# Performance work log

Measured on AMD Instinct MI355X. Metric: run time of the kernel, lower is better.

## Reference

```python
import jax, jax.numpy as jnp
import numpy as np

N_NODES = 100000
N_EDGES = 3200000
NFEAT = 256
NHID = 256
NOUT = 128


def setup_inputs() -> dict:
    key = jax.random.key(0)
    ks = jax.random.split(key, 8)
    stdv1 = 1.0 / np.sqrt(NHID)
    stdv2 = 1.0 / np.sqrt(NOUT)
    return {
        "feat": jax.random.normal(ks[0], (N_NODES, NFEAT), dtype=jnp.float32),
        "row": jax.random.randint(ks[1], (N_EDGES,), 0, N_NODES, dtype=jnp.int32),
        "col": jax.random.randint(ks[2], (N_EDGES,), 0, N_NODES, dtype=jnp.int32),
        "edge_weight": jax.random.uniform(ks[3], (N_EDGES,), dtype=jnp.float32),
        "W1": jax.random.uniform(ks[4], (NFEAT, NHID), jnp.float32, -stdv1, stdv1),
        "b1": jax.random.uniform(ks[5], (NHID,), jnp.float32, -stdv1, stdv1),
        "W2": jax.random.uniform(ks[6], (NHID, NOUT), jnp.float32, -stdv2, stdv2),
        "b2": jax.random.uniform(ks[7], (NOUT,), jnp.float32, -stdv2, stdv2),
    }


def _spmm(row, col, edge_weight, x, n_nodes):
    # sparse.mm(adj, x): out[i] = sum_e w[e] * x[col[e]] for row[e] == i
    msgs = x[col] * edge_weight[:, None]  # [E, F] gather + scale
    return jax.ops.segment_sum(msgs, row, num_segments=n_nodes)


def reference(feat, row, col, edge_weight, W1, b1, W2, b2):
    # Layer 1: GraphConvolution + ReLU (dropout is identity in eval mode)
    h = _spmm(row, col, edge_weight, feat @ W1, feat.shape[0]) + b1
    h = jax.nn.relu(h)
    # Layer 2: GraphConvolution (no activation on final layer)
    out = _spmm(row, col, edge_weight, h @ W2, feat.shape[0]) + b2
    return out
```

## Files before the change

### kernel.cpp

```cpp
#include <hip/hip_runtime.h>
#include <hip/hip_bf16.h>

#define M_NODES 100000
#define E_EDGES 3200000
#define NBUCK 196
#define BSHIFT 9
#define BCAP 24576
#define K3_EPB 8192
#define K3_BLOCKS 391
#define TILESM 391

typedef __attribute__((ext_vector_type(8))) short short8;
typedef __attribute__((ext_vector_type(4))) float f32x4;
typedef __attribute__((ext_vector_type(2))) float f32x2;

__device__ inline unsigned short f2bf(float f) {
  __hip_bfloat16 h = __float2bfloat16(f);
  return __builtin_bit_cast(unsigned short, h);
}

#if __has_builtin(__builtin_amdgcn_cvt_pk_f32_fp8) && __has_builtin(__builtin_amdgcn_cvt_pk_fp8_f32)
#define HW_FP8 1
#endif

#ifndef HW_FP8
__device__ inline float fp8_dec1(unsigned int b) {
  const unsigned int s = (b >> 7) & 1u, e = (b >> 3) & 15u, m = b & 7u;
  float v;
  if (e == 0) v = (float)m * 0.001953125f;
  else v = __uint_as_float(((e + 120u) << 23) | (m << 20));
  return s ? -v : v;
}
__device__ inline unsigned int fp8_enc1(float x) {
  const unsigned int sb = (__float_as_uint(x) >> 31) << 7;
  float ax = fminf(fabsf(x), 448.f);
  if (ax < 0.0009765625f) return sb;
  const unsigned int xb = __float_as_uint(ax);
  const int ef = (int)(xb >> 23) - 127;
  if (ef < -6) {
    unsigned int m = (unsigned int)(ax * 512.f + 0.5f);
    if (m > 7u) return sb | 0x08u;
    return sb | m;
  }
  unsigned int m3 = ((xb & 0x7FFFFFu) + 0x80000u) >> 20;
  unsigned int e4 = (unsigned int)(ef + 7);
  if (m3 == 8u) { m3 = 0u; e4 += 1u; }
  if (e4 >= 16u) { e4 = 15u; m3 = 6u; }
  return sb | (e4 << 3) | m3;
}
#endif

__device__ inline void fp8x4_dec(unsigned int v, float* o) {
#ifdef HW_FP8
  const f32x2 lo = __builtin_amdgcn_cvt_pk_f32_fp8((int)v, false);
  const f32x2 hi = __builtin_amdgcn_cvt_pk_f32_fp8((int)v, true);
  o[0] = lo[0]; o[1] = lo[1]; o[2] = hi[0]; o[3] = hi[1];
#else
  o[0] = fp8_dec1(v & 255u); o[1] = fp8_dec1((v >> 8) & 255u);
  o[2] = fp8_dec1((v >> 16) & 255u); o[3] = fp8_dec1(v >> 24);
#endif
}
__device__ inline unsigned short fp8x2_enc(float a, float b) {
#ifdef HW_FP8
  const int p = __builtin_amdgcn_cvt_pk_fp8_f32(a, b, 0, false);
  return (unsigned short)(p & 0xFFFF);
#else
  return (unsigned short)(fp8_enc1(a) | (fp8_enc1(b) << 8));
#endif
}

__device__ inline unsigned int epk_col(unsigned int p) { return p >> 15; }
__device__ inline float epk_w(unsigned int p) {
  return __uint_as_float((p & 0x7FFFu) << 16);
}

__device__ inline void pack_one(const float* __restrict__ W,
                                unsigned short* __restrict__ Bf,
                                int idx, int N) {
  const int lane = idx & 63;
  const int f = idx >> 6;
  const int ntile = f % (N >> 4);
  const int kstep = f / (N >> 4);
  const int k0 = (kstep << 5) + ((lane >> 4) << 3);
  const int n = (ntile << 4) + (lane & 15);
  ushort4 lo, hi;
  lo.x = f2bf(W[(size_t)(k0 + 0) * N + n]);
  lo.y = f2bf(W[(size_t)(k0 + 1) * N + n]);
  lo.z = f2bf(W[(size_t)(k0 + 2) * N + n]);
  lo.w = f2bf(W[(size_t)(k0 + 3) * N + n]);
  hi.x = f2bf(W[(size_t)(k0 + 4) * N + n]);
  hi.y = f2bf(W[(size_t)(k0 + 5) * N + n]);
  hi.z = f2bf(W[(size_t)(k0 + 6) * N + n]);
  hi.w = f2bf(W[(size_t)(k0 + 7) * N + n]);
  *(ushort4*)&Bf[(size_t)idx * 8] = lo;
  *(ushort4*)&Bf[(size_t)idx * 8 + 4] = hi;
}

__global__ __launch_bounds__(512) void prep_fused(
    const int* __restrict__ row, const int* __restrict__ col,
    const float* __restrict__ w, int* __restrict__ bcnt,
    int2* __restrict__ P,
    const float* __restrict__ W1, const float* __restrict__ W2,
    unsigned short* __restrict__ W1f, unsigned short* __restrict__ W2f)
{
  __shared__ int2 stage[K3_EPB];
  __shared__ unsigned char sb[K3_EPB];
  __shared__ int hist[NBUCK], cur[NBUCK], delta[NBUCK];
  __shared__ int buf[256];
  const int t = threadIdx.x;

  if (blockIdx.x >= K3_BLOCKS) {
    const int pb = blockIdx.x - K3_BLOCKS;
    if (pb < 16) pack_one(W1, W1f, pb * 512 + t, 256);
    else         pack_one(W2, W2f, (pb - 16) * 512 + t, 128);
    return;
  }

  const int e0 = blockIdx.x * K3_EPB;
  const int e1 = min(e0 + K3_EPB, E_EDGES);
  if (t < NBUCK) hist[t] = 0;
  __syncthreads();
  for (int i = e0 + t; i < e1; i += 512)
    atomicAdd(&hist[row[i] >> BSHIFT], 1);
  __syncthreads();
  int v = 0;
  if (t < 256) {
    v = (t < NBUCK) ? hist[t] : 0;
    buf[t] = v;
  }
  __syncthreads();
  for (int d = 1; d < 256; d <<= 1) {
    int x = 0;
    if (t < 256 && t >= d) x = buf[t - d];
    __syncthreads();
    if (t < 256) buf[t] += x;
    __syncthreads();
  }
  if (t < NBUCK) {
    const int excl = buf[t] - hist[t];
    cur[t] = excl;
    const int g = atomicAdd(&bcnt[t], hist[t]);
    delta[t] = (t * BCAP + g) - excl;
  }
  __syncthreads();
  for (int i = e0 + t; i < e1; i += 512) {
    const int r = row[i];
    const int b = r >> BSHIFT;
    const int pos = atomicAdd(&cur[b], 1);
    stage[pos] = make_int2(col[i] | ((r & 511) << 20), __float_as_int(w[i]));
    sb[pos] = (unsigned char)b;
  }
  __syncthreads();
  const int n = e1 - e0;
  for (int i = t; i < n; i += 512)
    P[delta[sb[i]] + i] = stage[i];
}

__global__ __launch_bounds__(512) void csr_gemm1_fused(
    const int* __restrict__ bcnt, const int2* __restrict__ P,
    int* __restrict__ offs, unsigned int* __restrict__ epk,
    const float* __restrict__ A_, const unsigned short* __restrict__ Bf,
    unsigned char* __restrict__ C)
{
  __shared__ __align__(16) char smem[8 * 16 * 132 * 4];
  const int t = threadIdx.x;

  if (blockIdx.x < NBUCK) {
    int* buf   = (int*)smem;
    int* rhist = buf + 256;
    int* rcur  = rhist + 512;
    int* wsum  = rcur + 512;
    const int b = blockIdx.x;
    if (t < 256) buf[t] = (t < NBUCK) ? bcnt[t] : 0;
    __syncthreads();
    for (int d = 1; d < 256; d <<= 1) {
      int x = 0;
      if (t < 256 && t >= d) x = buf[t - d];
      __syncthreads();
      if (t < 256) buf[t] += x;
      __syncthreads();
    }
    const int cnt = bcnt[b];
    const int dst0 = buf[b] - cnt;
    const int src0 = b * BCAP;
    const int row0 = b << BSHIFT;
    if (b == 0 && t == 0) offs[M_NODES] = E_EDGES;
    __syncthreads();
    rhist[t] = 0;
    __syncthreads();
    for (int i = t; i < cnt; i += 512)
      atomicAdd(&rhist[(P[src0 + i].x >> 20) & 511], 1);
    __syncthreads();
    const int lane = t & 63, wv = t >> 6;
    const int v = rhist[t];
    int inc = v;
#pragma unroll
    for (int d = 1; d < 64; d <<= 1) {
      const int x = __shfl_up(inc, d);
      if (lane >= d) inc += x;
    }
    if (lane == 63) wsum[wv] = inc;
    __syncthreads();
    if (t < 8) {
      int sv = wsum[t];
#pragma unroll
      for (int d = 1; d < 8; d <<= 1) {
        const int x = __shfl_up(sv, d);
        if ((int)t >= d) sv += x;
      }
      wsum[t] = sv;
    }
    __syncthreads();
    const int excl = (wv ? wsum[wv - 1] : 0) + inc - v;
    const int gofs = dst0 + excl;
    if (row0 + t < M_NODES) offs[row0 + t] = gofs;
    rcur[t] = gofs;
    __syncthreads();
    for (int i = t; i < cnt; i += 512) {
      const int2 p = P[src0 + i];
      const int rl = (p.x >> 20) & 511;
      const int pos = atomicAdd(&rcur[rl], 1);
      const unsigned int wb = (unsigned int)f2bf(__int_as_float(p.y));
      epk[pos] = (((unsigned int)p.x & 0xFFFFFu) << 15) | wb;
    }
    return;
  }

  float (*cbuf)[16][132] = reinterpret_cast<float (*)[16][132]>(smem);
  const int bm = blockIdx.x - NBUCK;
  const int wv = t >> 6, lane = t & 63;
  const int m0 = (bm << 8) + ((wv & 3) << 6);
  const int n0 = (wv >> 2) << 7;
  const int rif = lane & 15, kg = lane >> 4;

  f32x4 acc[4][8] = {};

#pragma unroll
  for (int ks = 0; ks < 8; ++ks) {
    const int k0 = (ks << 5) + (kg << 3);
    short8 bfr[8];
    const size_t fbase = ((size_t)(ks << 4) + (n0 >> 4)) * 64 + lane;
#pragma unroll
    for (int nf = 0; nf < 8; ++nf)
      bfr[nf] = *(const short8*)&Bf[(fbase + (size_t)nf * 64) * 8];

    short8 afr[4];
#pragma unroll
    for (int mi = 0; mi < 4; ++mi) {
      const int row = m0 + (mi << 4) + rif;
      if (row < M_NODES) {
        const float* ap = &A_[(size_t)row * 256 + k0];
        const float4 lo = *(const float4*)ap;
        const float4 hi = *(const float4*)(ap + 4);
        short8 tt;
        tt[0] = (short)f2bf(lo.x); tt[1] = (short)f2bf(lo.y);
        tt[2] = (short)f2bf(lo.z); tt[3] = (short)f2bf(lo.w);
        tt[4] = (short)f2bf(hi.x); tt[5] = (short)f2bf(hi.y);
        tt[6] = (short)f2bf(hi.z); tt[7] = (short)f2bf(hi.w);
        afr[mi] = tt;
      } else {
        afr[mi] = (short8)0;
      }
    }
#pragma unroll
    for (int mi = 0; mi < 4; ++mi)
#pragma unroll
      for (int nf = 0; nf < 8; ++nf)
        acc[mi][nf] = __builtin_amdgcn_mfma_f32_16x16x32_bf16(
            afr[mi], bfr[nf], acc[mi][nf], 0, 0, 0);
  }

#pragma unroll
  for (int mi = 0; mi < 4; ++mi) {
#pragma unroll
    for (int nf = 0; nf < 8; ++nf) {
#pragma unroll
      for (int r = 0; r < 4; ++r)
        cbuf[wv][(kg << 2) + r][(nf << 4) + rif] = acc[mi][nf][r];
    }
    __syncthreads();
#pragma unroll
    for (int r = 0; r < 16; ++r) {
      const int row = m0 + (mi << 4) + r;
      if (row < M_NODES) {
        const float2 v = *(const float2*)&cbuf[wv][r][lane << 1];
        *(unsigned short*)&C[(size_t)row * 256 + n0 + (lane << 1)] =
            fp8x2_enc(v.x, v.y);
      }
    }
    __syncthreads();
  }
}

__global__ __launch_bounds__(256) void gemm2_mfma(
    const unsigned short* __restrict__ A_, const unsigned short* __restrict__ Bf,
    unsigned char* __restrict__ C)
{
  __shared__ float cbuf[4][16][132];
  const int wv = threadIdx.x >> 6, lane = threadIdx.x & 63;
  const int m0 = (blockIdx.x << 8) + (wv << 6);
  const int rif = lane & 15, kg = lane >> 4;

  f32x4 acc[4][8] = {};

#pragma unroll
  for (int ks = 0; ks < 8; ++ks) {
    const int k0 = (ks << 5) + (kg << 3);
    short8 bfr[8];
    const size_t fbase = ((size_t)(ks << 3)) * 64 + lane;
#pragma unroll
    for (int nf = 0; nf < 8; ++nf)
      bfr[nf] = *(const short8*)&Bf[(fbase + (size_t)nf * 64) * 8];

    short8 afr[4];
#pragma unroll
    for (int mi = 0; mi < 4; ++mi) {
      const int row = m0 + (mi << 4) + rif;
      afr[mi] = (row < M_NODES)
          ? *(const short8*)&A_[(size_t)row * 256 + k0]
          : (short8)0;
    }
#pragma unroll
    for (int mi = 0; mi < 4; ++mi)
#pragma unroll
      for (int nf = 0; nf < 8; ++nf)
        acc[mi][nf] = __builtin_amdgcn_mfma_f32_16x16x32_bf16(
            afr[mi], bfr[nf], acc[mi][nf], 0, 0, 0);
  }

#pragma unroll
  for (int mi = 0; mi < 4; ++mi) {
#pragma unroll
    for (int nf = 0; nf < 8; ++nf) {
#pragma unroll
      for (int r = 0; r < 4; ++r)
        cbuf[wv][(kg << 2) + r][(nf << 4) + rif] = acc[mi][nf][r];
    }
    __syncthreads();
#pragma unroll
    for (int r = 0; r < 16; ++r) {
      const int row = m0 + (mi << 4) + r;
      if (row < M_NODES) {
        const float2 v = *(const float2*)&cbuf[wv][r][lane << 1];
        *(unsigned short*)&C[(size_t)row * 128 + (lane << 1)] =
            fp8x2_enc(v.x, v.y);
      }
    }
    __syncthreads();
  }
}

__global__ __launch_bounds__(256) void spmm1_fused(
    const int* __restrict__ offs, const unsigned int* __restrict__ epk,
    const unsigned char* __restrict__ X, const float* __restrict__ b1,
    unsigned short* __restrict__ Hb)
{
  const int w = threadIdx.x >> 6, lane = threadIdx.x & 63;
  const int half = lane >> 5, l5 = lane & 31;
  const int r = (blockIdx.x << 2) + w;
  const int s = offs[r], e = offs[r + 1];
  float a[8] = {};
  int i = s;
  for (; i + 8 <= e; i += 8) {
    unsigned int pe[4];
#pragma unroll
    for (int u = 0; u < 4; ++u) pe[u] = epk[i + (u << 1) + half];
    uint2 xv[4];
#pragma unroll
    for (int u = 0; u < 4; ++u)
      xv[u] = *(const uint2*)&X[((size_t)epk_col(pe[u]) << 8) + (l5 << 3)];
#pragma unroll
    for (int u = 0; u < 4; ++u) {
      const float wv = epk_w(pe[u]);
      float f[4], g[4];
      fp8x4_dec(xv[u].x, f);
      fp8x4_dec(xv[u].y, g);
      a[0] = fmaf(wv, f[0], a[0]); a[1] = fmaf(wv, f[1], a[1]);
      a[2] = fmaf(wv, f[2], a[2]); a[3] = fmaf(wv, f[3], a[3]);
      a[4] = fmaf(wv, g[0], a[4]); a[5] = fmaf(wv, g[1], a[5]);
      a[6] = fmaf(wv, g[2], a[6]); a[7] = fmaf(wv, g[3], a[7]);
    }
  }
  for (; i < e; i += 2) {
    const int idx = i + half;
    const unsigned int pe = (idx < e) ? epk[idx] : 0u;
    const float wv = (idx < e) ? epk_w(pe) : 0.f;
    const uint2 xw = *(const uint2*)&X[((size_t)epk_col(pe) << 8) + (l5 << 3)];
    float f[4], g[4];
    fp8x4_dec(xw.x, f);
    fp8x4_dec(xw.y, g);
    a[0] = fmaf(wv, f[0], a[0]); a[1] = fmaf(wv, f[1], a[1]);
    a[2] = fmaf(wv, f[2], a[2]); a[3] = fmaf(wv, f[3], a[3]);
    a[4] = fmaf(wv, g[0], a[4]); a[5] = fmaf(wv, g[1], a[5]);
    a[6] = fmaf(wv, g[2], a[6]); a[7] = fmaf(wv, g[3], a[7]);
  }
#pragma unroll
  for (int j = 0; j < 8; ++j) a[j] += __shfl_xor(a[j], 32);
  if (half == 0) {
    const float4 bv0 = *(const float4*)&b1[l5 << 3];
    const float4 bv1 = *(const float4*)&b1[(l5 << 3) + 4];
    short8 o;
    o[0] = (short)f2bf(fmaxf(a[0] + bv0.x, 0.f));
    o[1] = (short)f2bf(fmaxf(a[1] + bv0.y, 0.f));
    o[2] = (short)f2bf(fmaxf(a[2] + bv0.z, 0.f));
    o[3] = (short)f2bf(fmaxf(a[3] + bv0.w, 0.f));
    o[4] = (short)f2bf(fmaxf(a[4] + bv1.x, 0.f));
    o[5] = (short)f2bf(fmaxf(a[5] + bv1.y, 0.f));
    o[6] = (short)f2bf(fmaxf(a[6] + bv1.z, 0.f));
    o[7] = (short)f2bf(fmaxf(a[7] + bv1.w, 0.f));
    *(short8*)&Hb[((size_t)r << 8) + (l5 << 3)] = o;
  }
}

__global__ __launch_bounds__(256) void spmm2_quad(
    const int* __restrict__ offs, const unsigned int* __restrict__ epk,
    const unsigned char* __restrict__ X, const float* __restrict__ b2,
    float* __restrict__ Y)
{
  const int w = threadIdx.x >> 6, lane = threadIdx.x & 63;
  const int q = lane >> 4, l4 = lane & 15;
  const int r = (blockIdx.x << 2) + w;
  const int s = offs[r], e = offs[r + 1];
  float a[8] = {};
  int i = s;
  for (; i + 16 <= e; i += 16) {
    unsigned int pe[4];
#pragma unroll
    for (int u = 0; u < 4; ++u) pe[u] = epk[i + (u << 2) + q];
    uint2 xv[4];
#pragma unroll
    for (int u = 0; u < 4; ++u)
      xv[u] = *(const uint2*)&X[((size_t)epk_col(pe[u]) << 7) + (l4 << 3)];
#pragma unroll
    for (int u = 0; u < 4; ++u) {
      const float wv = epk_w(pe[u]);
      float f[4], g[4];
      fp8x4_dec(xv[u].x, f);
      fp8x4_dec(xv[u].y, g);
      a[0] = fmaf(wv, f[0], a[0]); a[1] = fmaf(wv, f[1], a[1]);
      a[2] = fmaf(wv, f[2], a[2]); a[3] = fmaf(wv, f[3], a[3]);
      a[4] = fmaf(wv, g[0], a[4]); a[5] = fmaf(wv, g[1], a[5]);
      a[6] = fmaf(wv, g[2], a[6]); a[7] = fmaf(wv, g[3], a[7]);
    }
  }
  for (; i < e; i += 4) {
    const int idx = i + q;
    const unsigned int pe = (idx < e) ? epk[idx] : 0u;
    const float wv = (idx < e) ? epk_w(pe) : 0.f;
    const uint2 xw = *(const uint2*)&X[((size_t)epk_col(pe) << 7) + (l4 << 3)];
    float f[4], g[4];
    fp8x4_dec(xw.x, f);
    fp8x4_dec(xw.y, g);
    a[0] = fmaf(wv, f[0], a[0]); a[1] = fmaf(wv, f[1], a[1]);
    a[2] = fmaf(wv, f[2], a[2]); a[3] = fmaf(wv, f[3], a[3]);
    a[4] = fmaf(wv, g[0], a[4]); a[5] = fmaf(wv, g[1], a[5]);
    a[6] = fmaf(wv, g[2], a[6]); a[7] = fmaf(wv, g[3], a[7]);
  }
#pragma unroll
  for (int j = 0; j < 8; ++j) {
    a[j] += __shfl_xor(a[j], 16);
    a[j] += __shfl_xor(a[j], 32);
  }
  if (q == 0) {
    const float4 bv0 = *(const float4*)&b2[l4 << 3];
    const float4 bv1 = *(const float4*)&b2[(l4 << 3) + 4];
    float* yp = &Y[((size_t)r << 7) + (l4 << 3)];
    *(float4*)yp = make_float4(a[0] + bv0.x, a[1] + bv0.y,
                               a[2] + bv0.z, a[3] + bv0.w);
    *(float4*)(yp + 4) = make_float4(a[4] + bv1.x, a[5] + bv1.y,
                                     a[6] + bv1.z, a[7] + bv1.w);
  }
}

extern "C" void kernel_launch(void* const* d_in, const int* in_sizes, int n_in,
                              void* d_out, int out_size, void* d_ws, size_t ws_size,
                              hipStream_t stream) {
  const float* feat = (const float*)d_in[0];
  const int*   row  = (const int*)d_in[1];
  const int*   col  = (const int*)d_in[2];
  const float* ew   = (const float*)d_in[3];
  const float* W1   = (const float*)d_in[4];
  const float* b1   = (const float*)d_in[5];
  const float* W2   = (const float*)d_in[6];
  const float* b2   = (const float*)d_in[7];
  float* out = (float*)d_out;

  unsigned short* Hb = (unsigned short*)d_ws;
  int2* P = (int2*)d_ws;
  unsigned char* X1 = (unsigned char*)(Hb + (size_t)M_NODES * 256);
  unsigned char* X2 = X1;
  unsigned int* epk = (unsigned int*)(X1 + (size_t)M_NODES * 256);
  int* offs  = (int*)(epk + E_EDGES);
  int* bcnt  = offs + 100004;
  unsigned short* W1f = (unsigned short*)(bcnt + 200);
  unsigned short* W2f = W1f + 65536;

  hipMemsetAsync(bcnt, 0, NBUCK * sizeof(int), stream);
  hipLaunchKernelGGL(prep_fused, dim3(K3_BLOCKS + 24), dim3(512), 0, stream,
                     row, col, ew, bcnt, P, W1, W2, W1f, W2f);
  hipLaunchKernelGGL(csr_gemm1_fused, dim3(NBUCK + TILESM), dim3(512), 0,
                     stream, bcnt, P, offs, epk, feat, W1f, X1);
  hipLaunchKernelGGL(spmm1_fused, dim3(M_NODES / 4), dim3(256), 0, stream,
                     offs, epk, X1, b1, Hb);
  hipLaunchKernelGGL(gemm2_mfma, dim3(TILESM), dim3(256), 0, stream,
                     (const unsigned short*)Hb, W2f, X2);
  hipLaunchKernelGGL(spmm2_quad, dim3(M_NODES / 4), dim3(256), 0, stream,
                     offs, epk, X2, b2, out);
}
```

Baseline: 337.2 us.

## Split prep and GEMM1 kernels, SoA edge staging, smaller XCD-aware GEMM1 blocks

Moves weight packing and the bucket-counter zeroing into a small separate kernel, which replaces the memset. Edge partitioning now writes separate column/row-key and weight arrays instead of int2 pairs. The fused GEMM1/CSR kernel drops from 512 to 256 threads, and each GEMM block now covers a 256x128 tile, so there are twice as many GEMM blocks. Those blocks are mapped to XCDs in an XCD-aware order, and CSR blocks handle two rows per thread. This aims to improve occupancy and L2 locality, at the cost of one extra kernel launch and more blocks.

```diff
diff --git a/kernel.cpp b/kernel.cpp
--- a/kernel.cpp
+++ b/kernel.cpp
@@ -9,6 +9,7 @@
 #define K3_EPB 8192
 #define K3_BLOCKS 391
 #define TILESM 391
+#define GEMM1_BLOCKS 784
 
 typedef __attribute__((ext_vector_type(8))) short short8;
 typedef __attribute__((ext_vector_type(4))) float f32x4;
@@ -96,26 +97,30 @@
   *(ushort4*)&Bf[(size_t)idx * 8 + 4] = hi;
 }
 
-__global__ __launch_bounds__(512) void prep_fused(
+__global__ __launch_bounds__(256) void pack_w_both(
+    const float* __restrict__ W1, const float* __restrict__ W2,
+    unsigned short* __restrict__ W1f, unsigned short* __restrict__ W2f,
+    int* __restrict__ bcnt)
+{
+  if (blockIdx.x < 32) {
+    pack_one(W1, W1f, blockIdx.x * 256 + threadIdx.x, 256);
+  } else if (blockIdx.x < 48) {
+    pack_one(W2, W2f, (blockIdx.x - 32) * 256 + threadIdx.x, 128);
+  } else {
+    if (threadIdx.x < NBUCK) bcnt[threadIdx.x] = 0;
+  }
+}
+
+__global__ __launch_bounds__(512) void partition_edges(
     const int* __restrict__ row, const int* __restrict__ col,
     const float* __restrict__ w, int* __restrict__ bcnt,
-    int2* __restrict__ P,
-    const float* __restrict__ W1, const float* __restrict__ W2,
-    unsigned short* __restrict__ W1f, unsigned short* __restrict__ W2f)
+    unsigned int* __restrict__ Px, unsigned int* __restrict__ Pw)
 {
   __shared__ int2 stage[K3_EPB];
   __shared__ unsigned char sb[K3_EPB];
   __shared__ int hist[NBUCK], cur[NBUCK], delta[NBUCK];
   __shared__ int buf[256];
   const int t = threadIdx.x;
-
-  if (blockIdx.x >= K3_BLOCKS) {
-    const int pb = blockIdx.x - K3_BLOCKS;
-    if (pb < 16) pack_one(W1, W1f, pb * 512 + t, 256);
-    else         pack_one(W2, W2f, (pb - 16) * 512 + t, 128);
-    return;
-  }
-
   const int e0 = blockIdx.x * K3_EPB;
   const int e1 = min(e0 + K3_EPB, E_EDGES);
   if (t < NBUCK) hist[t] = 0;
@@ -152,32 +157,36 @@
   }
   __syncthreads();
   const int n = e1 - e0;
-  for (int i = t; i < n; i += 512)
-    P[delta[sb[i]] + i] = stage[i];
-}
-
-__global__ __launch_bounds__(512) void csr_gemm1_fused(
-    const int* __restrict__ bcnt, const int2* __restrict__ P,
-    int* __restrict__ offs, unsigned int* __restrict__ epk,
+  for (int i = t; i < n; i += 512) {
+    const int d = delta[sb[i]] + i;
+    Px[d] = (unsigned int)stage[i].x;
+    Pw[d] = (unsigned int)stage[i].y;
+  }
+}
+
+__global__ __launch_bounds__(256) void gemm1_csr_fused(
     const float* __restrict__ A_, const unsigned short* __restrict__ Bf,
-    unsigned char* __restrict__ C)
+    unsigned char* __restrict__ C,
+    const int* __restrict__ bcnt, const unsigned int* __restrict__ Px,
+    const unsigned int* __restrict__ Pw, int* __restrict__ offs,
+    unsigned int* __restrict__ epk)
 {
-  __shared__ __align__(16) char smem[8 * 16 * 132 * 4];
+  __shared__ __align__(16) char smem[4 * 16 * 132 * 4];
   const int t = threadIdx.x;
 
-  if (blockIdx.x < NBUCK) {
+  if (blockIdx.x >= GEMM1_BLOCKS) {
     int* buf   = (int*)smem;
     int* rhist = buf + 256;
     int* rcur  = rhist + 512;
     int* wsum  = rcur + 512;
-    const int b = blockIdx.x;
-    if (t < 256) buf[t] = (t < NBUCK) ? bcnt[t] : 0;
+    const int b = blockIdx.x - GEMM1_BLOCKS;
+    buf[t] = (t < NBUCK) ? bcnt[t] : 0;
     __syncthreads();
     for (int d = 1; d < 256; d <<= 1) {
       int x = 0;
-      if (t < 256 && t >= d) x = buf[t - d];
+      if (t >= d) x = buf[t - d];
       __syncthreads();
-      if (t < 256) buf[t] += x;
+      buf[t] += x;
       __syncthreads();
     }
     const int cnt = bcnt[b];
@@ -187,13 +196,15 @@
     if (b == 0 && t == 0) offs[M_NODES] = E_EDGES;
     __syncthreads();
     rhist[t] = 0;
-    __syncthreads();
-    for (int i = t; i < cnt; i += 512)
-      atomicAdd(&rhist[(P[src0 + i].x >> 20) & 511], 1);
+    rhist[t + 256] = 0;
+    __syncthreads();
+    for (int i = t; i < cnt; i += 256)
+      atomicAdd(&rhist[(Px[src0 + i] >> 20) & 511], 1);
     __syncthreads();
     const int lane = t & 63, wv = t >> 6;
-    const int v = rhist[t];
-    int inc = v;
+    const int a0 = rhist[2 * t], a1 = rhist[2 * t + 1];
+    const int s = a0 + a1;
+    int inc = s;
 #pragma unroll
     for (int d = 1; d < 64; d <<= 1) {
       const int x = __shfl_up(inc, d);
@@ -201,36 +212,44 @@
     }
     if (lane == 63) wsum[wv] = inc;
     __syncthreads();
-    if (t < 8) {
+    if (t < 4) {
       int sv = wsum[t];
 #pragma unroll
-      for (int d = 1; d < 8; d <<= 1) {
+      for (int d = 1; d < 4; d <<= 1) {
         const int x = __shfl_up(sv, d);
         if ((int)t >= d) sv += x;
       }
       wsum[t] = sv;
     }
     __syncthreads();
-    const int excl = (wv ? wsum[wv - 1] : 0) + inc - v;
-    const int gofs = dst0 + excl;
-    if (row0 + t < M_NODES) offs[row0 + t] = gofs;
-    rcur[t] = gofs;
-    __syncthreads();
-    for (int i = t; i < cnt; i += 512) {
-      const int2 p = P[src0 + i];
-      const int rl = (p.x >> 20) & 511;
+    const int exclp = (wv ? wsum[wv - 1] : 0) + inc - s;
+    const int o0 = dst0 + exclp;
+    const int o1 = o0 + a0;
+    if (row0 + 2 * t < M_NODES) offs[row0 + 2 * t] = o0;
+    if (row0 + 2 * t + 1 < M_NODES) offs[row0 + 2 * t + 1] = o1;
+    rcur[2 * t] = o0;
+    rcur[2 * t + 1] = o1;
+    __syncthreads();
+    for (int i = t; i < cnt; i += 256) {
+      const unsigned int px = Px[src0 + i];
+      const unsigned int pw = Pw[src0 + i];
+      const int rl = (px >> 20) & 511;
       const int pos = atomicAdd(&rcur[rl], 1);
-      const unsigned int wb = (unsigned int)f2bf(__int_as_float(p.y));
-      epk[pos] = (((unsigned int)p.x & 0xFFFFFu) << 15) | wb;
+      const unsigned int wb = (unsigned int)f2bf(__uint_as_float(pw));
+      epk[pos] = ((px & 0xFFFFFu) << 15) | wb;
     }
     return;
   }
 
   float (*cbuf)[16][132] = reinterpret_cast<float (*)[16][132]>(smem);
-  const int bm = blockIdx.x - NBUCK;
   const int wv = t >> 6, lane = t & 63;
-  const int m0 = (bm << 8) + ((wv & 3) << 6);
-  const int n0 = (wv >> 2) << 7;
+  const int xcd = blockIdx.x & 7;
+  const int j = blockIdx.x >> 3;
+  const int bm = xcd * 49 + (j >> 1);
+  const int bn = j & 1;
+  if (bm >= TILESM) return;
+  const int m0 = (bm << 8) + (wv << 6);
+  const int n0 = bn << 7;
   const int rif = lane & 15, kg = lane >> 4;
 
   f32x4 acc[4][8] = {};
@@ -486,7 +505,8 @@
   float* out = (float*)d_out;
 
   unsigned short* Hb = (unsigned short*)d_ws;
-  int2* P = (int2*)d_ws;
+  unsigned int* Px = (unsigned int*)d_ws;
+  unsigned int* Pw = Px + (size_t)NBUCK * BCAP;
   unsigned char* X1 = (unsigned char*)(Hb + (size_t)M_NODES * 256);
   unsigned char* X2 = X1;
   unsigned int* epk = (unsigned int*)(X1 + (size_t)M_NODES * 256);
@@ -495,11 +515,12 @@
   unsigned short* W1f = (unsigned short*)(bcnt + 200);
   unsigned short* W2f = W1f + 65536;
 
-  hipMemsetAsync(bcnt, 0, NBUCK * sizeof(int), stream);
-  hipLaunchKernelGGL(prep_fused, dim3(K3_BLOCKS + 24), dim3(512), 0, stream,
-                     row, col, ew, bcnt, P, W1, W2, W1f, W2f);
-  hipLaunchKernelGGL(csr_gemm1_fused, dim3(NBUCK + TILESM), dim3(512), 0,
-                     stream, bcnt, P, offs, epk, feat, W1f, X1);
+  hipLaunchKernelGGL(pack_w_both, dim3(49), dim3(256), 0, stream,
+                     W1, W2, W1f, W2f, bcnt);
+  hipLaunchKernelGGL(partition_edges, dim3(K3_BLOCKS), dim3(512), 0, stream,
+                     row, col, ew, bcnt, Px, Pw);
+  hipLaunchKernelGGL(gemm1_csr_fused, dim3(GEMM1_BLOCKS + NBUCK), dim3(256), 0,
+                     stream, feat, W1f, X1, bcnt, Px, Pw, offs, epk);
   hipLaunchKernelGGL(spmm1_fused, dim3(M_NODES / 4), dim3(256), 0, stream,
                      offs, epk, X1, b1, Hb);
   hipLaunchKernelGGL(gemm2_mfma, dim3(TILESM), dim3(256), 0, stream,
```

Result: slower. 371.5 us (+10.2%).
